# Performance work log

Measured on AMD Instinct MI355X. Metric: run time of the kernel, lower is better.

## Reference

```python
import jax, jax.numpy as jnp
import numpy as np

N_NODES = 200000
N_EDGES = 3200000
N_FEAT = 165


def setup_inputs() -> dict:
    key = jax.random.key(0)
    ks = jax.random.split(key, 8)

    def glorot(k, fan_in, fan_out):
        lim = np.sqrt(6.0 / (fan_in + fan_out)).astype(np.float32)
        return jax.random.uniform(k, (fan_in, fan_out), jnp.float32, -lim, lim)

    x = jax.random.normal(ks[0], (N_NODES, N_FEAT), jnp.float32)
    edge_index = jax.random.randint(ks[1], (2, N_EDGES), 0, N_NODES, dtype=jnp.int64)
    return {
        "x": x,
        "edge_index": edge_index,
        "W1": glorot(ks[2], N_FEAT, 64), "b1": jnp.zeros((64,), jnp.float32),
        "W2": glorot(ks[3], 64, 16),     "b2": jnp.zeros((16,), jnp.float32),
        "W3": glorot(ks[4], 16, 2),      "b3": jnp.zeros((2,), jnp.float32),
    }


def _gcn_layer(x, src, dst, norm, W, b, n_nodes):
    # linear transform first (feature dim shrinks), then normalized scatter-add
    h = x @ W                                # [N, out]
    msg = h[src] * norm[:, None]             # gather over edges (incl. self-loops)
    out = jax.ops.segment_sum(msg, dst, num_segments=n_nodes)
    return out + b


def reference(x, edge_index, W1, b1, W2, b2, W3, b3):
    n = x.shape[0]
    loops = jnp.arange(n, dtype=edge_index.dtype)
    src = jnp.concatenate([edge_index[0], loops])   # PyG GCNConv adds self-loops
    dst = jnp.concatenate([edge_index[1], loops])
    # symmetric normalization deg^{-1/2}[src] * deg^{-1/2}[dst]
    deg = jax.ops.segment_sum(jnp.ones_like(dst, dtype=x.dtype), dst, num_segments=n)
    dinv = jnp.where(deg > 0, jax.lax.rsqrt(deg), 0.0)
    norm = dinv[src] * dinv[dst]                    # [E + N]

    h = jax.nn.relu(_gcn_layer(x, src, dst, norm, W1, b1, n))
    h = jax.nn.relu(_gcn_layer(h, src, dst, norm, W2, b2, n))
    h = _gcn_layer(h, src, dst, norm, W3, b3, n)
    return jax.nn.log_softmax(h, axis=1)
```

## Files before the change

### kernel.cpp

```cpp
#include <hip/hip_runtime.h>
#include <cstdint>
#include <math.h>

#define BLK 256
#define NBUK_MAX 1024

__device__ __forceinline__ float bf_lo(unsigned p) { return __uint_as_float(p << 16); }
__device__ __forceinline__ float bf_hi(unsigned p) { return __uint_as_float(p & 0xffff0000u); }
__device__ __forceinline__ unsigned pack2(float a, float b) {
  unsigned ua = __float_as_uint(a), ub = __float_as_uint(b);
  ua = (ua + 0x7fffu + ((ua >> 16) & 1u)) >> 16;
  ub = (ub + 0x7fffu + ((ub >> 16) & 1u)) >> 16;
  return (ua & 0xffffu) | (ub << 16);
}

typedef _Float16 half8 __attribute__((ext_vector_type(8)));
typedef float f32x4 __attribute__((ext_vector_type(4)));


__global__ void k_zero(int* __restrict__ p, int n) {
  int i = blockIdx.x * blockDim.x + threadIdx.x;
  if (i < n) p[i] = 0;
}


__global__ __launch_bounds__(BLK)
void k_bcount(const int* __restrict__ edges, long long E, long long chunk, int nbuk,
              int* __restrict__ bucket_counts) {
  __shared__ int hist[NBUK_MAX];
  for (int i = threadIdx.x; i < nbuk; i += BLK) hist[i] = 0;
  __syncthreads();
  long long beg = (long long)blockIdx.x * chunk;
  long long end = beg + chunk < E ? beg + chunk : E;
  for (long long e = beg + threadIdx.x; e < end; e += BLK)
    atomicAdd(&hist[edges[E + e] >> 8], 1);
  __syncthreads();
  for (int i = threadIdx.x; i < nbuk; i += BLK)
    if (hist[i]) atomicAdd(&bucket_counts[i], hist[i]);
}

__global__ __launch_bounds__(1024)
void k_bscan(const int* __restrict__ bucket_counts, int nbuk,
             int* __restrict__ bucket_start, int* __restrict__ bucket_cursor) {
  __shared__ int tmp[1024];
  int i = threadIdx.x;
  int v = (i < nbuk) ? bucket_counts[i] : 0;
  tmp[i] = v;
  __syncthreads();
  for (int off = 1; off < 1024; off <<= 1) {
    int t = (i >= off) ? tmp[i - off] : 0;
    __syncthreads();
    tmp[i] += t;
    __syncthreads();
  }
  if (i < nbuk) {
    int ex = tmp[i] - v;
    bucket_start[i] = ex;
    bucket_cursor[i] = ex;
  }
  if (i == nbuk - 1) bucket_start[nbuk] = tmp[i];
}

__global__ __launch_bounds__(BLK)
void k_bscatter(const int* __restrict__ edges, long long E, long long chunk, int nbuk,
                int* __restrict__ bucket_cursor, int* __restrict__ tmp_out) {
  __shared__ int hist[NBUK_MAX];
  __shared__ int base[NBUK_MAX];
  for (int i = threadIdx.x; i < nbuk; i += BLK) hist[i] = 0;
  __syncthreads();
  long long beg = (long long)blockIdx.x * chunk;
  long long end = beg + chunk < E ? beg + chunk : E;
  for (long long e = beg + threadIdx.x; e < end; e += BLK)
    atomicAdd(&hist[edges[E + e] >> 8], 1);
  __syncthreads();
  for (int i = threadIdx.x; i < nbuk; i += BLK) {
    int c = hist[i];
    base[i] = c ? atomicAdd(&bucket_cursor[i], c) : 0;
    hist[i] = 0;
  }
  __syncthreads();
  for (long long e = beg + threadIdx.x; e < end; e += BLK) {
    int s = edges[e];
    int d = edges[E + e];
    int b = d >> 8;
    int r = atomicAdd(&hist[b], 1);
    tmp_out[base[b] + r] = (s << 8) | (d & 255);
  }
}

__global__ __launch_bounds__(BLK)
void k_bfinal(const int* __restrict__ tmp_in, const int* __restrict__ bucket_start, int n,
              int* __restrict__ row_start, int* __restrict__ counts,
              float* __restrict__ dinv, int* __restrict__ col) {
  __shared__ int cnt[256];
  __shared__ int scan[256];
  __shared__ int cur[256];
  const int b = blockIdx.x, t = threadIdx.x;
  const int seg0 = bucket_start[b], seg1 = bucket_start[b + 1];
  cnt[t] = 0;
  __syncthreads();
  for (int i = seg0 + t; i < seg1; i += BLK) atomicAdd(&cnt[tmp_in[i] & 255], 1);
  __syncthreads();
  int v0 = cnt[t];
  scan[t] = v0;
  __syncthreads();
  for (int off = 1; off < 256; off <<= 1) {
    int x = (t >= off) ? scan[t - off] : 0;
    __syncthreads();
    scan[t] += x;
    __syncthreads();
  }
  int loff = scan[t] - v0;
  int v = b * 256 + t;
  if (v < n) {
    row_start[v] = seg0 + loff;
    counts[v] = v0;
    dinv[v] = rsqrtf((float)v0 + 1.0f);
  }
  cur[t] = loff;
  __syncthreads();
  for (int i = seg0 + t; i < seg1; i += BLK) {
    int p = tmp_in[i];
    int r = atomicAdd(&cur[p & 255], 1);
    col[seg0 + r] = p >> 8;
  }
}


__global__ __launch_bounds__(BLK)
void k_gemm1(const float* __restrict__ in, const float* __restrict__ W,
             const float* __restrict__ dinv, unsigned* __restrict__ hs1, int n) {
  __shared__ half8 Wl[6 * 4 * 64];
  const int t = threadIdx.x;
  const int lane = t & 63, w = t >> 6;

  for (int e = t; e < 12288; e += BLK) {
    int i = e & 7, ln = (e >> 3) & 63, cf = (e >> 9) & 3, ks = e >> 11;
    int k = ks * 32 + ((ln >> 4) << 3) + i;
    int c = (cf << 4) + (ln & 15);
    float v = (k < 165) ? W[k * 64 + c] : 0.f;
    ((_Float16*)Wl)[e] = (_Float16)v;
  }
  __syncthreads();

  const int row0 = blockIdx.x * 256 + w * 64;
  const int arow = row0 + (lane & 15);
  const int kg = (lane >> 4) << 3;

  f32x4 acc[4][4] = {};

  for (int ks = 0; ks < 6; ++ks) {
    half8 b0 = Wl[(ks * 4 + 0) * 64 + lane];
    half8 b1 = Wl[(ks * 4 + 1) * 64 + lane];
    half8 b2 = Wl[(ks * 4 + 2) * 64 + lane];
    half8 b3 = Wl[(ks * 4 + 3) * 64 + lane];
    const int kbase = ks * 32 + kg;
#pragma unroll
    for (int rf = 0; rf < 4; ++rf) {
      const int r = arow + rf * 16;
      float xv[8] = {0.f, 0.f, 0.f, 0.f, 0.f, 0.f, 0.f, 0.f};
      if (ks < 5) {
        if (r < n) {
          const float* p = in + (size_t)r * 165 + kbase;
#pragma unroll
          for (int i = 0; i < 8; ++i) xv[i] = p[i];
        }
      } else {
        if (r < n && kg == 0) {
          const float* p = in + (size_t)r * 165 + kbase;
#pragma unroll
          for (int i = 0; i < 5; ++i) xv[i] = p[i];
        }
      }
      half8 a;
#pragma unroll
      for (int i = 0; i < 8; ++i) a[i] = (_Float16)xv[i];
      acc[rf][0] = __builtin_amdgcn_mfma_f32_16x16x32_f16(a, b0, acc[rf][0], 0, 0, 0);
      acc[rf][1] = __builtin_amdgcn_mfma_f32_16x16x32_f16(a, b1, acc[rf][1], 0, 0, 0);
      acc[rf][2] = __builtin_amdgcn_mfma_f32_16x16x32_f16(a, b2, acc[rf][2], 0, 0, 0);
      acc[rf][3] = __builtin_amdgcn_mfma_f32_16x16x32_f16(a, b3, acc[rf][3], 0, 0, 0);
    }
  }

  const int cq = lane >> 4;
#pragma unroll
  for (int rf = 0; rf < 4; ++rf) {
    const int rb = row0 + rf * 16 + cq * 4;
    float4 dv4 = *(const float4*)&dinv[rb];
    float dvs[4] = {dv4.x, dv4.y, dv4.z, dv4.w};
#pragma unroll
    for (int j = 0; j < 4; ++j) {
      const int r = rb + j;
#pragma unroll
      for (int cf = 0; cf < 4; ++cf) {
        float v = acc[rf][cf][j] * dvs[j];
        float vn = __shfl_xor(v, 1);
        if (!(lane & 1) && r < n)
          hs1[(size_t)r * 32 + ((cf << 4) + (lane & 15)) / 2] = pack2(v, vn);
      }
    }
  }
}


#define W2S 33

__global__ __launch_bounds__(BLK)
void k_gather64g2(const unsigned* __restrict__ hs1, const int* __restrict__ row_start,
                  const int* __restrict__ counts, const int* __restrict__ col,
                  const float* __restrict__ dinv, const float* __restrict__ b1,
                  const float* __restrict__ W2, unsigned* __restrict__ hs2, int n) {
  __shared__ float W2l[64 * W2S];
  for (int i = threadIdx.x; i < 64 * 16; i += BLK)
    W2l[(i >> 4) * W2S + (i & 15)] = W2[i];
  __syncthreads();

  int wave = threadIdx.x >> 6, lane = threadIdx.x & 63;
  int v = blockIdx.x * 4 + wave;
  if (v >= n) return;
  int sub = lane >> 5, u = lane & 31;
  int beg = row_start[v], cnt = counts[v];

  float a0, a1;
  if (sub == 0) {
    unsigned p = hs1[(size_t)v * 32 + u];
    a0 = bf_lo(p); a1 = bf_hi(p);
  } else {
    a0 = 0.f; a1 = 0.f;
  }

  int e = sub;
  for (; e + 14 < cnt; e += 16) {
    int s0 = col[beg + e];
    int s1 = col[beg + e + 2];
    int s2 = col[beg + e + 4];
    int s3 = col[beg + e + 6];
    int s4 = col[beg + e + 8];
    int s5 = col[beg + e + 10];
    int s6 = col[beg + e + 12];
    int s7 = col[beg + e + 14];
    unsigned p0 = hs1[(size_t)s0 * 32 + u];
    unsigned p1 = hs1[(size_t)s1 * 32 + u];
    unsigned p2 = hs1[(size_t)s2 * 32 + u];
    unsigned p3 = hs1[(size_t)s3 * 32 + u];
    unsigned p4 = hs1[(size_t)s4 * 32 + u];
    unsigned p5 = hs1[(size_t)s5 * 32 + u];
    unsigned p6 = hs1[(size_t)s6 * 32 + u];
    unsigned p7 = hs1[(size_t)s7 * 32 + u];
    a0 += ((bf_lo(p0) + bf_lo(p1)) + (bf_lo(p2) + bf_lo(p3))) +
          ((bf_lo(p4) + bf_lo(p5)) + (bf_lo(p6) + bf_lo(p7)));
    a1 += ((bf_hi(p0) + bf_hi(p1)) + (bf_hi(p2) + bf_hi(p3))) +
          ((bf_hi(p4) + bf_hi(p5)) + (bf_hi(p6) + bf_hi(p7)));
  }
  for (; e + 6 < cnt; e += 8) {
    int s0 = col[beg + e];
    int s1 = col[beg + e + 2];
    int s2 = col[beg + e + 4];
    int s3 = col[beg + e + 6];
    unsigned p0 = hs1[(size_t)s0 * 32 + u];
    unsigned p1 = hs1[(size_t)s1 * 32 + u];
    unsigned p2 = hs1[(size_t)s2 * 32 + u];
    unsigned p3 = hs1[(size_t)s3 * 32 + u];
    a0 += (bf_lo(p0) + bf_lo(p1)) + (bf_lo(p2) + bf_lo(p3));
    a1 += (bf_hi(p0) + bf_hi(p1)) + (bf_hi(p2) + bf_hi(p3));
  }
  for (; e < cnt; e += 2) {
    unsigned p = hs1[(size_t)col[beg + e] * 32 + u];
    a0 += bf_lo(p); a1 += bf_hi(p);
  }
  a0 += __shfl_xor(a0, 32);
  a1 += __shfl_xor(a1, 32);

  float dv = dinv[v];
  float2 bb = ((const float2*)b1)[u];
  float r0 = fmaxf(fmaf(a0, dv, bb.x), 0.f);
  float r1 = fmaxf(fmaf(a1, dv, bb.y), 0.f);

  int o = lane & 15, q = lane >> 4;
  float part = 0.f;
#pragma unroll
  for (int i = 0; i < 16; i += 2) {
    int k = q * 16 + i;
    float e0 = __shfl(r0, k >> 1);
    float e1 = __shfl(r1, k >> 1);
    part = fmaf(e0, W2l[k * W2S + o], part);
    part = fmaf(e1, W2l[(k + 1) * W2S + o], part);
  }
  part += __shfl_xor(part, 16);
  part += __shfl_xor(part, 32);
  float h = part * dv;
  float hnext = __shfl_xor(h, 1);
  if (lane < 16 && (lane & 1) == 0)
    hs2[(size_t)v * 8 + (o >> 1)] = pack2(h, hnext);
}


__global__ __launch_bounds__(BLK)
void k_gather16g3(const unsigned* __restrict__ hs2, const int* __restrict__ row_start,
                  const int* __restrict__ counts, const int* __restrict__ col,
                  const float* __restrict__ dinv, const float* __restrict__ b2,
                  const float* __restrict__ W3, float* __restrict__ hs3, int n) {
  int wave = threadIdx.x >> 6, lane = threadIdx.x & 63;
  int v = blockIdx.x * 4 + wave;
  if (v >= n) return;
  int j = lane >> 3, p = lane & 7;
  int beg = row_start[v], cnt = counts[v];

  float a0 = 0.f, a1 = 0.f;
  int e = j;
  for (; e + 8 < cnt; e += 16) {
    unsigned pk0 = hs2[(size_t)col[beg + e] * 8 + p];
    unsigned pk1 = hs2[(size_t)col[beg + e + 8] * 8 + p];
    a0 += bf_lo(pk0) + bf_lo(pk1);
    a1 += bf_hi(pk0) + bf_hi(pk1);
  }
  if (e < cnt) {
    unsigned pk = hs2[(size_t)col[beg + e] * 8 + p];
    a0 += bf_lo(pk); a1 += bf_hi(pk);
  }
  a0 += __shfl_xor(a0, 8);  a1 += __shfl_xor(a1, 8);
  a0 += __shfl_xor(a0, 16); a1 += __shfl_xor(a1, 16);
  a0 += __shfl_xor(a0, 32); a1 += __shfl_xor(a1, 32);

  unsigned ps = hs2[(size_t)v * 8 + p];
  a0 += bf_lo(ps); a1 += bf_hi(ps);

  float dv = dinv[v];
  float2 bb = ((const float2*)b2)[p];
  float r0 = fmaxf(fmaf(a0, dv, bb.x), 0.f);
  float r1 = fmaxf(fmaf(a1, dv, bb.y), 0.f);

  int o = lane & 1;
  float part = 0.f;
#pragma unroll
  for (int i = 0; i < 8; ++i) {
    float e0 = __shfl(r0, i);
    float e1 = __shfl(r1, i);
    part = fmaf(e0, W3[(2 * i) * 2 + o], part);
    part = fmaf(e1, W3[(2 * i + 1) * 2 + o], part);
  }
  if (lane < 2) hs3[(size_t)v * 2 + o] = part * dv;
}


__global__ void k_gather2_lsm(const float* __restrict__ hs3, const int* __restrict__ row_start,
                              const int* __restrict__ counts, const int* __restrict__ col,
                              const float* __restrict__ dinv, const float* __restrict__ b,
                              float* __restrict__ out, int n) {
  int v = blockIdx.x * blockDim.x + threadIdx.x;
  if (v >= n) return;
  const float2* hs2v = (const float2*)hs3;
  int beg = row_start[v], cnt = counts[v];
  float2 self = hs2v[v];
  float a0 = self.x, a1 = self.y;
  for (int e = 0; e < cnt; ++e) {
    float2 m = hs2v[col[beg + e]];
    a0 += m.x;
    a1 += m.y;
  }
  float dv = dinv[v];
  a0 = fmaf(a0, dv, b[0]);
  a1 = fmaf(a1, dv, b[1]);
  float m = fmaxf(a0, a1);
  float l = m + logf(expf(a0 - m) + expf(a1 - m));
  out[2 * v] = a0 - l;
  out[2 * v + 1] = a1 - l;
}


extern "C" void kernel_launch(void* const* d_in, const int* in_sizes, int n_in,
                              void* d_out, int out_size, void* d_ws, size_t ws_size,
                              hipStream_t stream) {
  const float* x = (const float*)d_in[0];
  const int* edges = (const int*)d_in[1];
  const float* W1 = (const float*)d_in[2];
  const float* b1 = (const float*)d_in[3];
  const float* W2 = (const float*)d_in[4];
  const float* b2 = (const float*)d_in[5];
  const float* W3 = (const float*)d_in[6];
  const float* b3 = (const float*)d_in[7];
  float* out = (float*)d_out;

  const int N = in_sizes[0] / 165;
  const long long E = in_sizes[1] / 2;
  const int nbuk = (N + 255) >> 8;

  char* w = (char*)d_ws;
  int* counts        = (int*)w;  w += (size_t)N * 4;
  int* row_start     = (int*)w;  w += (size_t)N * 4;
  float* dinv        = (float*)w; w += (size_t)N * 4;
  int* bucket_counts = (int*)w;  w += (NBUK_MAX + 4) * 4;
  int* bucket_start  = (int*)w;  w += (NBUK_MAX + 4) * 4;
  int* bucket_cursor = (int*)w;  w += (NBUK_MAX + 4) * 4;
  int* col           = (int*)w;  w += (size_t)E * 4;
  unsigned* hs1      = (unsigned*)w; w += (size_t)N * 32 * 4;
  unsigned* hs2      = (unsigned*)w; w += (size_t)N * 8 * 4;
  float* hs3         = (float*)w;
  int* tmp = (int*)hs1;

  const int gN = (N + BLK - 1) / BLK;
  const int gW = (N + 3) / 4;
  const int NB_PART = 256;
  const long long chunk = (E + NB_PART - 1) / NB_PART;

  k_zero<<<(nbuk + BLK - 1) / BLK, BLK, 0, stream>>>(bucket_counts, nbuk);
  k_bcount<<<NB_PART, BLK, 0, stream>>>(edges, E, chunk, nbuk, bucket_counts);
  k_bscan<<<1, 1024, 0, stream>>>(bucket_counts, nbuk, bucket_start, bucket_cursor);
  k_bscatter<<<NB_PART, BLK, 0, stream>>>(edges, E, chunk, nbuk, bucket_cursor, tmp);
  k_bfinal<<<nbuk, BLK, 0, stream>>>(tmp, bucket_start, N, row_start, counts, dinv, col);

  k_gemm1<<<gN, BLK, 0, stream>>>(x, W1, dinv, hs1, N);

  k_gather64g2<<<gW, BLK, 0, stream>>>(hs1, row_start, counts, col, dinv, b1, W2, hs2, N);

  k_gather16g3<<<gW, BLK, 0, stream>>>(hs2, row_start, counts, col, dinv, b2, W3, hs3, N);

  k_gather2_lsm<<<gN, BLK, 0, stream>>>(hs3, row_start, counts, col, dinv, b3, out, N);
}
```

Baseline: 626.6 us.

## Stage X tile in LDS for gemm1 and split final gather across four lanes

The first GEMM now cooperatively loads a 128-row tile of x into shared memory as fp16 with coalesced reads, then feeds MFMA from LDS instead of doing strided per-lane global loads. Each block covers 128 rows rather than 256. The last gather plus log-softmax now uses four lanes per node, each taking every fourth edge, and reduces them with shuffles. This raises memory-level parallelism on the irregular gathers. It adds LDS pressure (about 42KB per block), which may limit occupancy.

```diff
diff --git a/kernel.cpp b/kernel.cpp
--- a/kernel.cpp
+++ b/kernel.cpp
@@ -127,12 +127,17 @@
 }
 
 
+#define G1R 128
+#define XPAD 168
+
 __global__ __launch_bounds__(BLK)
 void k_gemm1(const float* __restrict__ in, const float* __restrict__ W,
              const float* __restrict__ dinv, unsigned* __restrict__ hs1, int n) {
+  __shared__ _Float16 Xl[G1R * XPAD];
   __shared__ half8 Wl[6 * 4 * 64];
   const int t = threadIdx.x;
   const int lane = t & 63, w = t >> 6;
+  const int row0 = blockIdx.x * G1R;
 
   for (int e = t; e < 12288; e += BLK) {
     int i = e & 7, ln = (e >> 3) & 63, cf = (e >> 9) & 3, ks = e >> 11;
@@ -141,51 +146,52 @@
     float v = (k < 165) ? W[k * 64 + c] : 0.f;
     ((_Float16*)Wl)[e] = (_Float16)v;
   }
-  __syncthreads();
-
-  const int row0 = blockIdx.x * 256 + w * 64;
-  const int arow = row0 + (lane & 15);
+  {
+    const float* xb = in + (size_t)row0 * 165;
+    int lim = (n - row0) * 165;
+    if (lim > G1R * 165) lim = G1R * 165;
+    for (int idx = t; idx < G1R * 165; idx += BLK) {
+      float v = (idx < lim) ? xb[idx] : 0.f;
+      int r = idx / 165, k = idx - r * 165;
+      Xl[r * XPAD + k] = (_Float16)v;
+    }
+    for (int r = t; r < G1R; r += BLK) {
+      Xl[r * XPAD + 165] = (_Float16)0.f;
+      Xl[r * XPAD + 166] = (_Float16)0.f;
+      Xl[r * XPAD + 167] = (_Float16)0.f;
+    }
+  }
+  __syncthreads();
+
+  const int rl = (lane & 15);
   const int kg = (lane >> 4) << 3;
 
-  f32x4 acc[4][4] = {};
+  f32x4 acc[2][4] = {};
 
   for (int ks = 0; ks < 6; ++ks) {
     half8 b0 = Wl[(ks * 4 + 0) * 64 + lane];
     half8 b1 = Wl[(ks * 4 + 1) * 64 + lane];
     half8 b2 = Wl[(ks * 4 + 2) * 64 + lane];
     half8 b3 = Wl[(ks * 4 + 3) * 64 + lane];
-    const int kbase = ks * 32 + kg;
-#pragma unroll
-    for (int rf = 0; rf < 4; ++rf) {
-      const int r = arow + rf * 16;
-      float xv[8] = {0.f, 0.f, 0.f, 0.f, 0.f, 0.f, 0.f, 0.f};
-      if (ks < 5) {
-        if (r < n) {
-          const float* p = in + (size_t)r * 165 + kbase;
-#pragma unroll
-          for (int i = 0; i < 8; ++i) xv[i] = p[i];
-        }
-      } else {
-        if (r < n && kg == 0) {
-          const float* p = in + (size_t)r * 165 + kbase;
-#pragma unroll
-          for (int i = 0; i < 5; ++i) xv[i] = p[i];
-        }
-      }
-      half8 a;
-#pragma unroll
-      for (int i = 0; i < 8; ++i) a[i] = (_Float16)xv[i];
-      acc[rf][0] = __builtin_amdgcn_mfma_f32_16x16x32_f16(a, b0, acc[rf][0], 0, 0, 0);
-      acc[rf][1] = __builtin_amdgcn_mfma_f32_16x16x32_f16(a, b1, acc[rf][1], 0, 0, 0);
-      acc[rf][2] = __builtin_amdgcn_mfma_f32_16x16x32_f16(a, b2, acc[rf][2], 0, 0, 0);
-      acc[rf][3] = __builtin_amdgcn_mfma_f32_16x16x32_f16(a, b3, acc[rf][3], 0, 0, 0);
+    half8 a0 = {}, a1 = {};
+    if (ks < 5 || kg == 0) {
+      a0 = *(const half8*)&Xl[(w * 32 + rl) * XPAD + ks * 32 + kg];
+      a1 = *(const half8*)&Xl[(w * 32 + 16 + rl) * XPAD + ks * 32 + kg];
     }
+    acc[0][0] = __builtin_amdgcn_mfma_f32_16x16x32_f16(a0, b0, acc[0][0], 0, 0, 0);
+    acc[0][1] = __builtin_amdgcn_mfma_f32_16x16x32_f16(a0, b1, acc[0][1], 0, 0, 0);
+    acc[0][2] = __builtin_amdgcn_mfma_f32_16x16x32_f16(a0, b2, acc[0][2], 0, 0, 0);
+    acc[0][3] = __builtin_amdgcn_mfma_f32_16x16x32_f16(a0, b3, acc[0][3], 0, 0, 0);
+    acc[1][0] = __builtin_amdgcn_mfma_f32_16x16x32_f16(a1, b0, acc[1][0], 0, 0, 0);
+    acc[1][1] = __builtin_amdgcn_mfma_f32_16x16x32_f16(a1, b1, acc[1][1], 0, 0, 0);
+    acc[1][2] = __builtin_amdgcn_mfma_f32_16x16x32_f16(a1, b2, acc[1][2], 0, 0, 0);
+    acc[1][3] = __builtin_amdgcn_mfma_f32_16x16x32_f16(a1, b3, acc[1][3], 0, 0, 0);
   }
 
   const int cq = lane >> 4;
 #pragma unroll
-  for (int rf = 0; rf < 4; ++rf) {
-    const int rb = row0 + rf * 16 + cq * 4;
+  for (int rf = 0; rf < 2; ++rf) {
+    const int rb = row0 + w * 32 + rf * 16 + cq * 4;
     float4 dv4 = *(const float4*)&dinv[rb];
     float dvs[4] = {dv4.x, dv4.y, dv4.z, dv4.w};
 #pragma unroll
@@ -343,28 +349,43 @@
 }
 
 
-__global__ void k_gather2_lsm(const float* __restrict__ hs3, const int* __restrict__ row_start,
-                              const int* __restrict__ counts, const int* __restrict__ col,
-                              const float* __restrict__ dinv, const float* __restrict__ b,
-                              float* __restrict__ out, int n) {
-  int v = blockIdx.x * blockDim.x + threadIdx.x;
+__global__ __launch_bounds__(BLK)
+void k_gather2_lsm(const float* __restrict__ hs3, const int* __restrict__ row_start,
+                   const int* __restrict__ counts, const int* __restrict__ col,
+                   const float* __restrict__ dinv, const float* __restrict__ b,
+                   float* __restrict__ out, int n) {
+  int t = threadIdx.x;
+  int v = blockIdx.x * 64 + (t >> 2);
+  int sl = t & 3;
   if (v >= n) return;
-  const float2* hs2v = (const float2*)hs3;
+  const float2* h = (const float2*)hs3;
   int beg = row_start[v], cnt = counts[v];
-  float2 self = hs2v[v];
-  float a0 = self.x, a1 = self.y;
-  for (int e = 0; e < cnt; ++e) {
-    float2 m = hs2v[col[beg + e]];
-    a0 += m.x;
-    a1 += m.y;
-  }
-  float dv = dinv[v];
-  a0 = fmaf(a0, dv, b[0]);
-  a1 = fmaf(a1, dv, b[1]);
-  float m = fmaxf(a0, a1);
-  float l = m + logf(expf(a0 - m) + expf(a1 - m));
-  out[2 * v] = a0 - l;
-  out[2 * v + 1] = a1 - l;
+  float a0 = 0.f, a1 = 0.f;
+  int e = sl;
+  for (; e + 4 < cnt; e += 8) {
+    int c0 = col[beg + e];
+    int c1 = col[beg + e + 4];
+    float2 m0 = h[c0];
+    float2 m1 = h[c1];
+    a0 += m0.x + m1.x;
+    a1 += m0.y + m1.y;
+  }
+  if (e < cnt) {
+    float2 m = h[col[beg + e]];
+    a0 += m.x; a1 += m.y;
+  }
+  a0 += __shfl_xor(a0, 1); a1 += __shfl_xor(a1, 1);
+  a0 += __shfl_xor(a0, 2); a1 += __shfl_xor(a1, 2);
+  if (sl == 0) {
+    float2 self = h[v];
+    a0 += self.x; a1 += self.y;
+    float dv = dinv[v];
+    a0 = fmaf(a0, dv, b[0]);
+    a1 = fmaf(a1, dv, b[1]);
+    float m = fmaxf(a0, a1);
+    float l = m + logf(expf(a0 - m) + expf(a1 - m));
+    ((float2*)out)[v] = make_float2(a0 - l, a1 - l);
+  }
 }
 
 
@@ -409,11 +430,11 @@
   k_bscatter<<<NB_PART, BLK, 0, stream>>>(edges, E, chunk, nbuk, bucket_cursor, tmp);
   k_bfinal<<<nbuk, BLK, 0, stream>>>(tmp, bucket_start, N, row_start, counts, dinv, col);
 
-  k_gemm1<<<gN, BLK, 0, stream>>>(x, W1, dinv, hs1, N);
+  k_gemm1<<<(N + G1R - 1) / G1R, BLK, 0, stream>>>(x, W1, dinv, hs1, N);
 
   k_gather64g2<<<gW, BLK, 0, stream>>>(hs1, row_start, counts, col, dinv, b1, W2, hs2, N);
 
   k_gather16g3<<<gW, BLK, 0, stream>>>(hs2, row_start, counts, col, dinv, b2, W3, hs3, N);
 
-  k_gather2_lsm<<<gN, BLK, 0, stream>>>(hs3, row_start, counts, col, dinv, b3, out, N);
-}
+  k_gather2_lsm<<<(N + 63) / 64, BLK, 0, stream>>>(hs3, row_start, counts, col, dinv, b3, out, N);
+}
```

After: 753.9 us. +20.3%, slower.
